# Kernel tuning notes

Hardware: AMD Instinct MI355X
Metric: run time of the kernel (lower is better)

Reference implementation:

```python
import jax, jax.numpy as jnp
import numpy as np

D_MODEL = 1024
N_HEADS = 16
D_K = D_MODEL // N_HEADS
NEG_INF = -1e30


def setup_inputs() -> dict:
    key = jax.random.key(0)
    ks = jax.random.split(key, 12)
    B, S = 4, 2048
    scale = 1.0 / np.sqrt(D_MODEL)
    inp = {
        "query": jax.random.normal(ks[0], (B, S, D_MODEL), jnp.float32),
        "key": jax.random.normal(ks[1], (B, S, D_MODEL), jnp.float32),
        "value": jax.random.normal(ks[2], (B, S, D_MODEL), jnp.float32),
        "mask": jax.random.randint(ks[3], (B, S, S), 0, 2, jnp.int32),
        "w_q": jax.random.normal(ks[4], (D_MODEL, D_MODEL), jnp.float32) * scale,
        "b_q": jnp.zeros((D_MODEL,), jnp.float32),
        "w_k": jax.random.normal(ks[5], (D_MODEL, D_MODEL), jnp.float32) * scale,
        "b_k": jnp.zeros((D_MODEL,), jnp.float32),
        "w_v": jax.random.normal(ks[6], (D_MODEL, D_MODEL), jnp.float32) * scale,
        "b_v": jnp.zeros((D_MODEL,), jnp.float32),
        "w_o": jax.random.normal(ks[7], (D_MODEL, D_MODEL), jnp.float32) * scale,
        "b_o": jnp.zeros((D_MODEL,), jnp.float32),
    }
    return inp


def reference(query, key, value, mask, w_q, b_q, w_k, b_k, w_v, b_v, w_o, b_o):
    B, Sq, _ = query.shape
    Sk = key.shape[1]
    # Linear projections (torch nn.Linear: x @ W.T + b), split into heads
    Q = (query @ w_q.T + b_q).reshape(B, Sq, N_HEADS, D_K).transpose(0, 2, 1, 3)
    K = (key @ w_k.T + b_k).reshape(B, Sk, N_HEADS, D_K).transpose(0, 2, 1, 3)
    V = (value @ w_v.T + b_v).reshape(B, Sk, N_HEADS, D_K).transpose(0, 2, 1, 3)
    # scores: (B, H, Sq, Sk)
    scores = jnp.einsum('bhqd,bhkd->bhqk', Q, K) / jnp.sqrt(jnp.float32(D_K))
    scores = jnp.where(mask[:, None, :, :] == 0, NEG_INF, scores)
    attn = jax.nn.softmax(scores, axis=-1)  # dropout p=0 -> identity (eval)
    context = jnp.einsum('bhqk,bhkd->bhqd', attn, V)
    context = context.transpose(0, 2, 1, 3).reshape(B, Sq, D_MODEL)
    return context @ w_o.T + b_o
```

## Files before the change

kernel.cpp:

```cpp
#include <hip/hip_runtime.h>
#include <hip/hip_bf16.h>
#include <stdint.h>

#define DM 1024
#define NHEADS 16
#define DK 64
#define BB 4
#define SS 2048

typedef unsigned short u16;
typedef __bf16 bf16x8 __attribute__((ext_vector_type(8)));
typedef __bf16 bf16x4 __attribute__((ext_vector_type(4)));
typedef float f32x4 __attribute__((ext_vector_type(4)));

#if __has_builtin(__builtin_amdgcn_exp2f)
#define EXP2(x) __builtin_amdgcn_exp2f(x)
#else
#define EXP2(x) exp2f(x)
#endif

static __device__ __forceinline__ u16 f2bf(float f) {
    union { float f; uint32_t u; } v; v.f = f;
    uint32_t r = v.u + 0x7fffu + ((v.u >> 16) & 1u);
    return (u16)(r >> 16);
}

static __device__ __forceinline__ f32x4 mfma16(bf16x8 a, bf16x8 b, f32x4 c) {
    return __builtin_amdgcn_mfma_f32_16x16x32_bf16(a, b, c, 0, 0, 0);
}

static __device__ __forceinline__ void gload16(const u16* g, u16* l) {
    __builtin_amdgcn_global_load_lds((const __attribute__((address_space(1))) void*)g,
                                     (__attribute__((address_space(3))) void*)l, 16, 0, 0);
}

#define PREP_W 4096
#define PREP_X 12288
#define PREP_M 2048
__global__ __launch_bounds__(256) void k_prep(const float* __restrict__ wq, const float* __restrict__ wk,
                                              const float* __restrict__ wv, const float* __restrict__ wo,
                                              u16* __restrict__ wout,
                                              const float* __restrict__ xq, const float* __restrict__ xk,
                                              const float* __restrict__ xv, u16* __restrict__ xout,
                                              const int* __restrict__ mask, uint32_t* __restrict__ bits) {
    const int bid = blockIdx.x, tid = threadIdx.x;
    if (bid < PREP_W) {
        int t = bid * 256 + tid;
        int which = t >> 18;
        int off = (t & 0x3FFFF) << 2;
        const float* src = (which == 0) ? wq : (which == 1) ? wk : (which == 2) ? wv : wo;
        float4 v = *(const float4*)(src + off);
        ushort4 o;
        o.x = f2bf(v.x); o.y = f2bf(v.y); o.z = f2bf(v.z); o.w = f2bf(v.w);
        *(ushort4*)(wout + ((size_t)which << 20) + off) = o;
    } else if (bid < PREP_W + PREP_X) {
        int lb = bid - PREP_W;
        int which = lb >> 12;
        const float* src = (which == 0) ? xq : (which == 1) ? xk : xv;
        size_t base = (((size_t)(lb & 4095)) * 256 + tid) * 8;
        float4 v0 = *(const float4*)(src + base);
        float4 v1 = *(const float4*)(src + base + 4);
        union { u16 s[8]; uint4 u; } p;
        p.s[0]=f2bf(v0.x); p.s[1]=f2bf(v0.y); p.s[2]=f2bf(v0.z); p.s[3]=f2bf(v0.w);
        p.s[4]=f2bf(v1.x); p.s[5]=f2bf(v1.y); p.s[6]=f2bf(v1.z); p.s[7]=f2bf(v1.w);
        *(uint4*)(xout + ((size_t)which << 23) + base) = p.u;
    } else {
        int lb = bid - PREP_W - PREP_X;
        int gid = lb * 256 + tid;
        int lane = gid & 63;
        int wv_ = gid >> 6;
        const int nw = (PREP_M * 256) >> 6;
        const long totalInts = (long)BB * SS * SS;
        for (long base = (long)wv_ * 64; base < totalInts; base += (long)nw * 64) {
            int m = mask[base + lane];
            unsigned long long bal = __ballot(m != 0);
            if (lane == 0)  bits[(base >> 5)]     = (uint32_t)bal;
            if (lane == 32) bits[(base >> 5) + 1] = (uint32_t)(bal >> 32);
        }
    }
}

__global__ __launch_bounds__(256) void k_projqkv(const u16* __restrict__ Xq, const u16* __restrict__ Xk,
                                                 const u16* __restrict__ Xv, const u16* __restrict__ Wb,
                                                 const float* __restrict__ bq, const float* __restrict__ bk,
                                                 const float* __restrict__ bv,
                                                 u16* __restrict__ Qw, u16* __restrict__ Kw,
                                                 u16* __restrict__ Vw, float qscale) {
    __shared__ u16 Ab[128 * 32];
    __shared__ u16 Bb[128 * 32];
    const int sel = blockIdx.x >> 9;
    const int tile = blockIdx.x & 511;
    const u16* X = (sel == 0) ? Xq : (sel == 1) ? Xk : Xv;
    const u16* W = Wb + ((size_t)sel << 20);
    const float* bias = (sel == 0) ? bq : (sel == 1) ? bk : bv;
    u16* Y = (sel == 0) ? Qw : (sel == 1) ? Kw : Vw;
    const float alpha = (sel == 0) ? qscale : 1.0f;

    const int tid = threadIdx.x;
    const int lane = tid & 63, wv = tid >> 6;
    const int wr = wv >> 1, wc = wv & 1;
    const int lrow = lane & 15, lgrp = lane >> 4;
    const int m0 = (tile >> 3) * 128;
    const int n0 = (tile & 7) * 128;
    const int trow = tid >> 2;
    const int tk = (tid & 3) * 8;

    f32x4 acc[4][4] = {};

    for (int kk = 0; kk < DM; kk += 32) {
#pragma unroll
        for (int i = 0; i < 2; ++i) {
            gload16(X + (size_t)(m0 + i * 64 + trow) * DM + kk + tk, &Ab[(i * 256 + tid) * 8]);
            gload16(W + (size_t)(n0 + i * 64 + trow) * DM + kk + tk, &Bb[(i * 256 + tid) * 8]);
        }
        __syncthreads();
        bf16x8 af[4], bfr[4];
#pragma unroll
        for (int i = 0; i < 4; ++i)
            af[i] = *(const bf16x8*)&Ab[(wr * 64 + i * 16 + lrow) * 32 + lgrp * 8];
#pragma unroll
        for (int j = 0; j < 4; ++j)
            bfr[j] = *(const bf16x8*)&Bb[(wc * 64 + j * 16 + lrow) * 32 + lgrp * 8];
#pragma unroll
        for (int i = 0; i < 4; ++i)
#pragma unroll
            for (int j = 0; j < 4; ++j)
                acc[i][j] = mfma16(af[i], bfr[j], acc[i][j]);
        __syncthreads();
    }

#pragma unroll
    for (int j = 0; j < 4; ++j) {
        int n = n0 + wc * 64 + j * 16 + lrow;
        float bv_ = bias[n];
        int h = n >> 6, d = n & 63;
#pragma unroll
        for (int i = 0; i < 4; ++i) {
            int mbase = m0 + wr * 64 + i * 16 + (lgrp << 2);
            if (sel != 2) {
#pragma unroll
                for (int r = 0; r < 4; ++r) {
                    int m = mbase + r;
                    int b = m >> 11, s = m & 2047;
                    Y[(((size_t)(b * NHEADS + h) * SS) + s) * DK + d] = f2bf((acc[i][j][r] + bv_) * alpha);
                }
            } else {
                int b = mbase >> 11, s = mbase & 2047;
                ushort4 o;
                o.x = f2bf(acc[i][j][0] + bv_);
                o.y = f2bf(acc[i][j][1] + bv_);
                o.z = f2bf(acc[i][j][2] + bv_);
                o.w = f2bf(acc[i][j][3] + bv_);
                *(ushort4*)&Y[(((size_t)(b * NHEADS + h) * DK) + d) * SS + s] = o;
            }
        }
    }
}

__global__ __launch_bounds__(256) void k_oproj(const u16* __restrict__ X, const u16* __restrict__ W,
                                               const float* __restrict__ bias, float* __restrict__ out) {
    __shared__ u16 Ab[128 * 32];
    __shared__ u16 Bb[128 * 32];
    const int tid = threadIdx.x;
    const int lane = tid & 63, wv = tid >> 6;
    const int wr = wv >> 1, wc = wv & 1;
    const int lrow = lane & 15, lgrp = lane >> 4;
    const int m0 = (blockIdx.x >> 3) * 128;
    const int n0 = (blockIdx.x & 7) * 128;
    const int trow = tid >> 2;
    const int tk = (tid & 3) * 8;

    f32x4 acc[4][4] = {};

    for (int kk = 0; kk < DM; kk += 32) {
#pragma unroll
        for (int i = 0; i < 2; ++i) {
            gload16(X + (size_t)(m0 + i * 64 + trow) * DM + kk + tk, &Ab[(i * 256 + tid) * 8]);
            gload16(W + (size_t)(n0 + i * 64 + trow) * DM + kk + tk, &Bb[(i * 256 + tid) * 8]);
        }
        __syncthreads();
        bf16x8 af[4], bfr[4];
#pragma unroll
        for (int i = 0; i < 4; ++i)
            af[i] = *(const bf16x8*)&Ab[(wr * 64 + i * 16 + lrow) * 32 + lgrp * 8];
#pragma unroll
        for (int j = 0; j < 4; ++j)
            bfr[j] = *(const bf16x8*)&Bb[(wc * 64 + j * 16 + lrow) * 32 + lgrp * 8];
#pragma unroll
        for (int i = 0; i < 4; ++i)
#pragma unroll
            for (int j = 0; j < 4; ++j)
                acc[i][j] = mfma16(af[i], bfr[j], acc[i][j]);
        __syncthreads();
    }

#pragma unroll
    for (int j = 0; j < 4; ++j) {
        int n = n0 + wc * 64 + j * 16 + lrow;
        float bv = bias[n];
#pragma unroll
        for (int i = 0; i < 4; ++i) {
            int mbase = m0 + wr * 64 + i * 16 + (lgrp << 2);
#pragma unroll
            for (int r = 0; r < 4; ++r)
                out[(size_t)(mbase + r) * DM + n] = acc[i][j][r] + bv;
        }
    }
}

#define NT (SS / 64)
__global__ __launch_bounds__(512, 4) void k_attn(const u16* __restrict__ Q, const u16* __restrict__ K,
                                                 const u16* __restrict__ VT, const uint32_t* __restrict__ mbits,
                                                 u16* __restrict__ ctx) {
    __shared__ u16 Kt[2][64 * 64];
    __shared__ u16 Vt[2][64 * 64];
    __shared__ u16 Pl[8][16][72];
    const int tid = threadIdx.x;
    const int lane = tid & 63, w = tid >> 6;
    const int lrow = lane & 15, lgrp = lane >> 4;
    const int bid = blockIdx.x;
    const int bh = bid & 63;
    const int qt = bid >> 6;
    const int b = bh >> 4, h = bh & 15;
    const int qbase = qt * 128 + w * 16;

    const u16* Qh = Q + (size_t)bh * SS * DK;
    const u16* Kh = K + (size_t)bh * SS * DK;
    const u16* Vh = VT + (size_t)bh * DK * SS;

    bf16x8 qf0, qf1;
    {
        const u16* p = Qh + (size_t)(qbase + lrow) * DK + lgrp * 8;
        qf0 = *(const bf16x8*)(p);
        qf1 = *(const bf16x8*)(p + 32);
    }

    const uint64_t* mrow = (const uint64_t*)mbits + ((size_t)(b * SS + qbase + lrow)) * (SS / 64);

    union { uint4 u; bf16x8 v; } onesu;
    onesu.u = make_uint4(0x3F803F80u, 0x3F803F80u, 0x3F803F80u, 0x3F803F80u);
    const bf16x8 ones = onesu.v;

    const int swzA = (lgrp * 8) ^ ((lrow & 7) * 8);
    const int swzB = (32 + lgrp * 8) ^ ((lrow & 7) * 8);

    const int srow = tid >> 3;
    const int ssrc = ((tid & 7) * 8) ^ ((srow & 7) * 8);

    f32x4 acc[4] = {};
    f32x4 asum = {};

    gload16(Kh + (size_t)srow * DK + ssrc, &Kt[0][tid * 8]);
    gload16(Vh + (size_t)srow * SS + ssrc, &Vt[0][tid * 8]);
    __syncthreads();

    int cur = 0;
    for (int kt = 0; kt < NT; ++kt) {
        if (kt + 1 < NT) {
            gload16(Kh + (size_t)((kt + 1) * 64 + srow) * DK + ssrc, &Kt[cur ^ 1][tid * 8]);
            gload16(Vh + (size_t)srow * SS + (kt + 1) * 64 + ssrc, &Vt[cur ^ 1][tid * 8]);
        }
        const uint64_t wm = mrow[kt];

        const u16* Kc = Kt[cur];
        const u16* Vc = Vt[cur];
        f32x4 st[4] = {};
#pragma unroll
        for (int t = 0; t < 4; ++t) {
            bf16x8 ka = *(const bf16x8*)&Kc[(16 * t + lrow) * 64 + swzA];
            bf16x8 kb = *(const bf16x8*)&Kc[(16 * t + lrow) * 64 + swzB];
            st[t] = mfma16(ka, qf0, st[t]);
            st[t] = mfma16(kb, qf1, st[t]);
        }
#pragma unroll
        for (int t = 0; t < 4; ++t) {
            uint32_t wt = (uint32_t)(wm >> (16 * t + 4 * lgrp));
            bf16x4 pk;
#pragma unroll
            for (int r = 0; r < 4; ++r) {
                float p = EXP2(st[t][r]);
                p = ((wt >> r) & 1u) ? p : 0.0f;
                pk[r] = (__bf16)p;
            }
            *(bf16x4*)&Pl[w][lrow][16 * t + 4 * lgrp] = pk;
        }
        bf16x8 pf0 = *(const bf16x8*)&Pl[w][lrow][lgrp * 8];
        bf16x8 pf1 = *(const bf16x8*)&Pl[w][lrow][32 + lgrp * 8];
        asum = mfma16(pf0, ones, asum);
        asum = mfma16(pf1, ones, asum);
#pragma unroll
        for (int dt = 0; dt < 4; ++dt) {
            bf16x8 vf0 = *(const bf16x8*)&Vc[(16 * dt + lrow) * 64 + swzA];
            bf16x8 vf1 = *(const bf16x8*)&Vc[(16 * dt + lrow) * 64 + swzB];
            acc[dt] = mfma16(pf0, vf0, acc[dt]);
            acc[dt] = mfma16(pf1, vf1, acc[dt]);
        }
        __syncthreads();
        cur ^= 1;
    }

#pragma unroll
    for (int r = 0; r < 4; ++r) {
        float li = 1.0f / asum[r];
        int q = qbase + 4 * lgrp + r;
#pragma unroll
        for (int dt = 0; dt < 4; ++dt)
            ctx[((size_t)b * SS + q) * DM + h * 64 + dt * 16 + lrow] = f2bf(acc[dt][r] * li);
    }
}

extern "C" void kernel_launch(void* const* d_in, const int* in_sizes, int n_in,
                              void* d_out, int out_size, void* d_ws, size_t ws_size,
                              hipStream_t stream) {
    const float* query = (const float*)d_in[0];
    const float* key   = (const float*)d_in[1];
    const float* value = (const float*)d_in[2];
    const int*   mask  = (const int*)d_in[3];
    const float* w_q   = (const float*)d_in[4];
    const float* b_q   = (const float*)d_in[5];
    const float* w_k   = (const float*)d_in[6];
    const float* b_k   = (const float*)d_in[7];
    const float* w_v   = (const float*)d_in[8];
    const float* b_v   = (const float*)d_in[9];
    const float* w_o   = (const float*)d_in[10];
    const float* b_o   = (const float*)d_in[11];
    float* out = (float*)d_out;

    char* ws = (char*)d_ws;
    u16*      Wb = (u16*)(ws);
    uint32_t* mb = (uint32_t*)(ws + (8u  << 20));
    u16*      Xq = (u16*)(ws + (16u << 20));
    u16*      Xk = (u16*)(ws + (32u << 20));
    u16*      Xv = (u16*)(ws + (48u << 20));
    u16*      Qw = (u16*)(ws + (64u << 20));
    u16*      Kw = (u16*)(ws + (80u << 20));
    u16*      Vw = (u16*)(ws + (96u << 20));
    u16*      Cw = (u16*)(ws + (112u << 20));

    const float qscale = 0.125f * 1.4426950408889634f;

    k_prep<<<dim3(PREP_W + PREP_X + PREP_M), dim3(256), 0, stream>>>(
        w_q, w_k, w_v, w_o, Wb, query, key, value, Xq, mask, mb);
    k_projqkv<<<dim3(1536), dim3(256), 0, stream>>>(Xq, Xk, Xv, Wb, b_q, b_k, b_v,
                                                    Qw, Kw, Vw, qscale);
    k_attn<<<dim3(1024), dim3(512), 0, stream>>>(Qw, Kw, Vw, mb, Cw);
    k_oproj<<<dim3(512), dim3(256), 0, stream>>>(Cw, Wb + (3u << 20), b_o, out);
}
```

Measured before the change: 278.2 us.

## Triple-buffer K/V tiles and overlap next QK^T with current PV

Switches the attention kernel's K/V shared-memory staging from double to triple buffering, prefetching two tiles ahead. The score MFMAs for the next key tile are issued in the same phase as the PV MFMAs for the current tile, and the mask word is fetched one iteration early. The aim is to hide global-load latency and the exp/pack step behind matrix work. The larger LDS footprint may cut the number of resident blocks per CU.

```diff
diff --git a/kernel.cpp b/kernel.cpp
--- a/kernel.cpp
+++ b/kernel.cpp
@@ -212,8 +212,8 @@
 __global__ __launch_bounds__(512, 4) void k_attn(const u16* __restrict__ Q, const u16* __restrict__ K,
                                                  const u16* __restrict__ VT, const uint32_t* __restrict__ mbits,
                                                  u16* __restrict__ ctx) {
-    __shared__ u16 Kt[2][64 * 64];
-    __shared__ u16 Vt[2][64 * 64];
+    __shared__ u16 Kt[3][64 * 64];
+    __shared__ u16 Vt[3][64 * 64];
     __shared__ u16 Pl[8][16][72];
     const int tid = threadIdx.x;
     const int lane = tid & 63, w = tid >> 6;
@@ -252,26 +252,26 @@
 
     gload16(Kh + (size_t)srow * DK + ssrc, &Kt[0][tid * 8]);
     gload16(Vh + (size_t)srow * SS + ssrc, &Vt[0][tid * 8]);
+    gload16(Kh + (size_t)(64 + srow) * DK + ssrc, &Kt[1][tid * 8]);
+    gload16(Vh + (size_t)srow * SS + 64 + ssrc, &Vt[1][tid * 8]);
     __syncthreads();
 
+    f32x4 st[4];
+#pragma unroll
+    for (int t = 0; t < 4; ++t) {
+        f32x4 z = {};
+        bf16x8 ka = *(const bf16x8*)&Kt[0][(16 * t + lrow) * 64 + swzA];
+        bf16x8 kb = *(const bf16x8*)&Kt[0][(16 * t + lrow) * 64 + swzB];
+        z = mfma16(ka, qf0, z);
+        z = mfma16(kb, qf1, z);
+        st[t] = z;
+    }
+
+    uint64_t wm = mrow[0];
     int cur = 0;
     for (int kt = 0; kt < NT; ++kt) {
-        if (kt + 1 < NT) {
-            gload16(Kh + (size_t)((kt + 1) * 64 + srow) * DK + ssrc, &Kt[cur ^ 1][tid * 8]);
-            gload16(Vh + (size_t)srow * SS + (kt + 1) * 64 + ssrc, &Vt[cur ^ 1][tid * 8]);
-        }
-        const uint64_t wm = mrow[kt];
-
-        const u16* Kc = Kt[cur];
-        const u16* Vc = Vt[cur];
-        f32x4 st[4] = {};
-#pragma unroll
-        for (int t = 0; t < 4; ++t) {
-            bf16x8 ka = *(const bf16x8*)&Kc[(16 * t + lrow) * 64 + swzA];
-            bf16x8 kb = *(const bf16x8*)&Kc[(16 * t + lrow) * 64 + swzB];
-            st[t] = mfma16(ka, qf0, st[t]);
-            st[t] = mfma16(kb, qf1, st[t]);
-        }
+        const int nxt = (cur == 2) ? 0 : cur + 1;
+        const int nx2 = (nxt == 2) ? 0 : nxt + 1;
 #pragma unroll
         for (int t = 0; t < 4; ++t) {
             uint32_t wt = (uint32_t)(wm >> (16 * t + 4 * lgrp));
@@ -285,18 +285,39 @@
             *(bf16x4*)&Pl[w][lrow][16 * t + 4 * lgrp] = pk;
         }
         bf16x8 pf0 = *(const bf16x8*)&Pl[w][lrow][lgrp * 8];
-        bf16x8 pf1 = *(const bf16x8*)&Pl[w][lrow][32 + lgrp * 8];
+        bf16x8 pf1 = *(const bf16x8*)&Pl[w][lrow][32 + 8 * lgrp];
         asum = mfma16(pf0, ones, asum);
         asum = mfma16(pf1, ones, asum);
-#pragma unroll
-        for (int dt = 0; dt < 4; ++dt) {
-            bf16x8 vf0 = *(const bf16x8*)&Vc[(16 * dt + lrow) * 64 + swzA];
-            bf16x8 vf1 = *(const bf16x8*)&Vc[(16 * dt + lrow) * 64 + swzB];
-            acc[dt] = mfma16(pf0, vf0, acc[dt]);
-            acc[dt] = mfma16(pf1, vf1, acc[dt]);
-        }
-        __syncthreads();
-        cur ^= 1;
+        __syncthreads();
+        if (kt + 2 < NT) {
+            gload16(Kh + (size_t)((kt + 2) * 64 + srow) * DK + ssrc, &Kt[nx2][tid * 8]);
+            gload16(Vh + (size_t)srow * SS + (kt + 2) * 64 + ssrc, &Vt[nx2][tid * 8]);
+        }
+        f32x4 stn[4] = {};
+        if (kt + 1 < NT) {
+            const u16* Kn = &Kt[nxt][0];
+#pragma unroll
+            for (int t = 0; t < 4; ++t) {
+                bf16x8 ka = *(const bf16x8*)&Kn[(16 * t + lrow) * 64 + swzA];
+                bf16x8 kb = *(const bf16x8*)&Kn[(16 * t + lrow) * 64 + swzB];
+                stn[t] = mfma16(ka, qf0, stn[t]);
+                stn[t] = mfma16(kb, qf1, stn[t]);
+            }
+        }
+        {
+            const u16* Vc = &Vt[cur][0];
+#pragma unroll
+            for (int dt = 0; dt < 4; ++dt) {
+                bf16x8 vf0 = *(const bf16x8*)&Vc[(16 * dt + lrow) * 64 + swzA];
+                bf16x8 vf1 = *(const bf16x8*)&Vc[(16 * dt + lrow) * 64 + swzB];
+                acc[dt] = mfma16(pf0, vf0, acc[dt]);
+                acc[dt] = mfma16(pf1, vf1, acc[dt]);
+            }
+        }
+        if (kt + 1 < NT) wm = mrow[kt + 1];
+#pragma unroll
+        for (int t = 0; t < 4; ++t) st[t] = stn[t];
+        cur = nxt;
     }
 
 #pragma unroll
```

Result: no change. 273.6 us (-1.7%).
